# Kernel tuning notes

Hardware: AMD Instinct MI355X
Metric: run time of the kernel (lower is better)

The kernel has to match this reference:

```python
import jax, jax.numpy as jnp
import numpy as np

N_NODES = 100000
N_EDGES = 1600000
N_ADJS = 2
N_LAYERS = 3
D_IN = 128
H = 128           # hidden dim; last conv out = 256 / num_adjs = 128
N_GRAPHS = 1024


def setup_inputs() -> dict:
    key = jax.random.key(0)
    ks = jax.random.split(key, 12)
    x = jax.random.normal(ks[0], (N_NODES, D_IN), dtype=jnp.float32)
    edge_index = jax.random.randint(ks[1], (N_ADJS, 2, N_EDGES), 0, N_NODES, dtype=jnp.int32)
    batch = jnp.sort(jax.random.randint(ks[2], (N_NODES,), 0, N_GRAPHS, dtype=jnp.int32))
    s = 0.05
    lin0_w = jax.random.normal(ks[3], (D_IN, H), dtype=jnp.float32) * s
    lin0_b = jnp.zeros((H,), dtype=jnp.float32)
    conv_w = jax.random.normal(ks[4], (N_ADJS, N_LAYERS, H, H), dtype=jnp.float32) * s
    lin1_w = jax.random.normal(ks[5], (2 * H, H), dtype=jnp.float32) * s
    lin1_b = jnp.zeros((H,), dtype=jnp.float32)
    lin2_w = jax.random.normal(ks[6], (H, 1), dtype=jnp.float32) * s
    lin2_b = jnp.zeros((1,), dtype=jnp.float32)
    return {"x": x, "edge_index": edge_index, "batch": batch,
            "lin0_w": lin0_w, "lin0_b": lin0_b, "conv_w": conv_w,
            "lin1_w": lin1_w, "lin1_b": lin1_b, "lin2_w": lin2_w, "lin2_b": lin2_b}


def _gcn_conv(h, W, row, col, norm, n_nodes):
    # GCNConv (bias=False): out[i] = sum_{j->i} norm_e * (h @ W)[j]
    m = h @ W                                  # [N, H] dense transform first (PyG order)
    msg = m[row] * norm[:, None]               # [E+N, H] gather + edge scaling
    return jax.ops.segment_sum(msg, col, num_segments=n_nodes)


def reference(x, edge_index, batch, lin0_w, lin0_b, conv_w, lin1_w, lin1_b, lin2_w, lin2_b):
    n = x.shape[0]
    loops = jnp.arange(n, dtype=edge_index.dtype)
    x0 = jax.nn.relu(x @ lin0_w + lin0_b)      # lin0 + relu
    pooled = []
    for a in range(N_ADJS):
        # gcn_norm with self loops: deg over targets, norm = d^-1/2[row] * d^-1/2[col]
        row = jnp.concatenate([edge_index[a, 0], loops])
        col = jnp.concatenate([edge_index[a, 1], loops])
        deg = jax.ops.segment_sum(jnp.ones_like(col, dtype=x.dtype), col, num_segments=n)
        dis = jnp.where(deg > 0, jax.lax.rsqrt(jnp.maximum(deg, 1e-12)), 0.0)
        norm = dis[row] * dis[col]
        h = x0
        for l in range(N_LAYERS):
            h = jax.nn.relu(_gcn_conv(h, conv_w[a, l], row, col, norm, n))
        # global_add_pool: segment sum over graph ids
        pooled.append(jax.ops.segment_sum(h, batch, num_segments=N_GRAPHS))
    g = jnp.concatenate(pooled, axis=1)        # [G, 256]
    g = jax.nn.relu(g @ lin1_w + lin1_b)
    # dropout(p=0.5) is identity in eval mode
    return g @ lin2_w + lin2_b                 # [G, 1]
```

## Files before the change

kernel.cpp:

```cpp
#include <hip/hip_runtime.h>

#define NN 100000
#define NE 1600000
#define NADJ 2
#define NLAY 3
#define HD 128
#define NG 1024

#define EB   1563
#define NBUK 391
#define BPAD 400

typedef unsigned int uint32;
typedef unsigned short u16;

typedef __attribute__((ext_vector_type(8))) short bfrag8;
typedef __attribute__((ext_vector_type(4))) float f32x4;
typedef __attribute__((ext_vector_type(2))) float f32x2;

__device__ __forceinline__ u16 f2bf(float f) {
    uint32 u = __float_as_uint(f);
    u += 0x7FFFu + ((u >> 16) & 1u);
    return (u16)(u >> 16);
}
__device__ __forceinline__ float bflo(uint32 u) { return __uint_as_float(u << 16); }
__device__ __forceinline__ float bfhi(uint32 u) { return __uint_as_float(u & 0xFFFF0000u); }

__global__ __launch_bounds__(256) void to_bf16(const float* __restrict__ in,
                                               u16* __restrict__ o) {
    int i = blockIdx.x * 256 + threadIdx.x;
    float4 a = ((const float4*)in)[i * 2];
    float4 b = ((const float4*)in)[i * 2 + 1];
    uint4 v;
    v.x = (uint32)f2bf(a.x) | ((uint32)f2bf(a.y) << 16);
    v.y = (uint32)f2bf(a.z) | ((uint32)f2bf(a.w) << 16);
    v.z = (uint32)f2bf(b.x) | ((uint32)f2bf(b.y) << 16);
    v.w = (uint32)f2bf(b.z) | ((uint32)f2bf(b.w) << 16);
    ((uint4*)o)[i] = v;
}

__global__ void wt_prep(const float* __restrict__ conv_w,
                        const float* __restrict__ lin0_w, u16* __restrict__ wt) {
    const float* W = (blockIdx.x < 6) ? conv_w + (size_t)blockIdx.x * HD * HD
                                      : lin0_w;
    u16* o = wt + (size_t)blockIdx.x * HD * HD;
    for (int i = 0; i < 64; ++i) {
        int idx = i * 256 + threadIdx.x;
        int n = idx >> 7, k = idx & 127;
        o[idx] = f2bf(W[k * 128 + n]);
    }
}

__global__ __launch_bounds__(256) void gemm_mfma(
    const u16* __restrict__ Abf, const u16* __restrict__ Wt,
    u16* __restrict__ outbf, const float* __restrict__ dis,
    const float* __restrict__ bias, int relu)
{
    const int wid = blockIdx.x * 4 + (threadIdx.x >> 6);
    const int lane = threadIdx.x & 63;
    const int row0 = (wid >> 1) * 64;
    if (row0 >= NN) return;
    const int wc = (wid & 1) * 64;
    const int lr = lane & 15, kg = lane >> 4;

    bfrag8 b[4][4];
    #pragma unroll
    for (int ks = 0; ks < 4; ++ks)
        #pragma unroll
        for (int j = 0; j < 4; ++j)
            b[ks][j] = *(const bfrag8*)&Wt[(size_t)(wc + j * 16 + lr) * 128
                                           + (ks * 4 + kg) * 8];

    const f32x4 z = {0.f, 0.f, 0.f, 0.f};
    f32x4 acc[4][4];
    #pragma unroll
    for (int i = 0; i < 4; ++i)
        #pragma unroll
        for (int j = 0; j < 4; ++j) acc[i][j] = z;

    #pragma unroll
    for (int ks = 0; ks < 4; ++ks) {
        bfrag8 a[4];
        #pragma unroll
        for (int i = 0; i < 4; ++i) {
            int r = min(row0 + i * 16 + lr, NN - 1);
            a[i] = *(const bfrag8*)&Abf[(size_t)r * 128 + (ks * 4 + kg) * 8];
        }
        #pragma unroll
        for (int i = 0; i < 4; ++i)
            #pragma unroll
            for (int j = 0; j < 4; ++j)
                acc[i][j] = __builtin_amdgcn_mfma_f32_16x16x32_bf16(
                    a[i], b[ks][j], acc[i][j], 0, 0, 0);
    }

    #pragma unroll
    for (int i = 0; i < 4; ++i) {
        #pragma unroll
        for (int r = 0; r < 4; ++r) {
            int grow = row0 + i * 16 + kg * 4 + r;
            if (grow < NN) {
                float ds = dis ? dis[grow] : 1.f;
                #pragma unroll
                for (int j = 0; j < 4; ++j) {
                    int gcol = wc + j * 16 + lr;
                    float o = acc[i][j][r] * ds;
                    if (bias) o += bias[gcol];
                    if (relu) o = fmaxf(o, 0.f);
                    outbf[(size_t)grow * 128 + gcol] = f2bf(o);
                }
            }
        }
    }
}


__global__ __launch_bounds__(256) void p1_count(
    const int* __restrict__ col, int* __restrict__ bcnt)
{
    __shared__ int h[NBUK];
    int t = threadIdx.x;
    for (int q = t; q < NBUK; q += 256) h[q] = 0;
    __syncthreads();
    int base = blockIdx.x * 1024 + t;
    #pragma unroll
    for (int u = 0; u < 4; ++u) {
        int e = base + u * 256;
        if (e < NE) atomicAdd(&h[col[e] >> 8], 1);
    }
    __syncthreads();
    for (int q = t; q < NBUK; q += 256)
        bcnt[blockIdx.x * BPAD + q] = h[q];
}

__global__ __launch_bounds__(256) void p2a_scanblocks(
    const int* __restrict__ bcnt, int* __restrict__ pscan,
    int* __restrict__ btot)
{
    __shared__ int s[256];
    int b = blockIdx.x;
    int t = threadIdx.x;
    int v[7];
    int loc = 0;
    #pragma unroll
    for (int j = 0; j < 7; ++j) {
        int idx = t * 7 + j;
        v[j] = (idx < EB) ? bcnt[idx * BPAD + b] : 0;
        loc += v[j];
    }
    s[t] = loc;
    __syncthreads();
    for (int off = 1; off < 256; off <<= 1) {
        int u = (t >= off) ? s[t - off] : 0;
        __syncthreads();
        s[t] += u;
        __syncthreads();
    }
    int pre = s[t] - loc;
    #pragma unroll
    for (int j = 0; j < 7; ++j) {
        int idx = t * 7 + j;
        if (idx < EB) pscan[idx * BPAD + b] = pre;
        pre += v[j];
    }
    if (t == 255) btot[b] = s[255];
}

__global__ __launch_bounds__(512) void p2b_scanbuckets(
    const int* __restrict__ btot, int* __restrict__ bbase)
{
    __shared__ int s[512];
    int t = threadIdx.x;
    int v = (t < NBUK) ? btot[t] : 0;
    s[t] = v;
    __syncthreads();
    for (int off = 1; off < 512; off <<= 1) {
        int u = (t >= off) ? s[t - off] : 0;
        __syncthreads();
        s[t] += u;
        __syncthreads();
    }
    if (t < NBUK) bbase[t] = s[t] - v;
    if (t == NBUK - 1) bbase[NBUK] = s[t];
}

__global__ __launch_bounds__(256) void p3_partition(
    const int* __restrict__ row, const int* __restrict__ col,
    const int* __restrict__ pscan, const int* __restrict__ bbase,
    uint2* __restrict__ part)
{
    __shared__ int spre[NBUK];
    __shared__ int cur[NBUK];
    int t = threadIdx.x;
    for (int q = t; q < NBUK; q += 256) {
        spre[q] = bbase[q] + pscan[blockIdx.x * BPAD + q];
        cur[q] = 0;
    }
    __syncthreads();
    int base = blockIdx.x * 1024 + t;
    #pragma unroll
    for (int u = 0; u < 4; ++u) {
        int e = base + u * 256;
        if (e < NE) {
            int c = col[e];
            int b = c >> 8;
            int rk = atomicAdd(&cur[b], 1);
            part[spre[b] + rk] = make_uint2((uint32)row[e], (uint32)c);
        }
    }
}

__global__ __launch_bounds__(256) void p4_csr(
    const uint2* __restrict__ part, const int* __restrict__ bbase,
    int* __restrict__ row_ptr, float* __restrict__ dis,
    int* __restrict__ csr_src)
{
    __shared__ int cnt[256];
    __shared__ int s[256];
    __shared__ int sexcl[256];
    __shared__ int cur[256];
    int b = blockIdx.x, t = threadIdx.x;
    int base = bbase[b];
    int ecnt = bbase[b + 1] - base;
    int n0 = b << 8;
    cnt[t] = 0;
    cur[t] = 0;
    __syncthreads();
    for (int i = t; i < ecnt; i += 256)
        atomicAdd(&cnt[part[base + i].y - n0], 1);
    __syncthreads();
    int v = cnt[t];
    s[t] = v;
    __syncthreads();
    for (int off = 1; off < 256; off <<= 1) {
        int u = (t >= off) ? s[t - off] : 0;
        __syncthreads();
        s[t] += u;
        __syncthreads();
    }
    sexcl[t] = s[t] - v;
    int node = n0 + t;
    if (node < NN) {
        row_ptr[node] = base + s[t] - v;
        dis[node] = rsqrtf((float)(v + 1));
    }
    if (b == 0 && t == 0) row_ptr[NN] = NE;
    __syncthreads();
    for (int i = t; i < ecnt; i += 256) {
        uint2 p = part[base + i];
        int li = (int)p.y - n0;
        int rk = atomicAdd(&cur[li], 1);
        csr_src[base + sexcl[li] + rk] = (int)p.x;
    }
}

__global__ __launch_bounds__(256) void agg_relu(
    const u16* __restrict__ mm, const int* __restrict__ row_ptr,
    const int* __restrict__ csr_src,
    const float* __restrict__ dis, u16* __restrict__ out)
{
    int wid = blockIdx.x * 4 + (threadIdx.x >> 6);
    int nodeA = wid * 2;
    if (nodeA >= NN) return;
    int nodeB = nodeA + 1;
    uint32 lane = threadIdx.x & 63;
    const uint32* mv = (const uint32*)mm;
    int lan16 = (int)(lane & 15);

    uint32 selfA = mv[(uint32)nodeA * 64u + lane];
    uint32 selfB = mv[(uint32)nodeB * 64u + lane];
    f32x2 accA, accB;
    accA.x = bflo(selfA); accA.y = bfhi(selfA);
    accB.x = bflo(selfB); accB.y = bfhi(selfB);
    int eA = row_ptr[nodeA], e1A = row_ptr[nodeA + 1];
    int eB = e1A,            e1B = row_ptr[nodeB + 1];

    while (eA + 16 <= e1A && eB + 16 <= e1B) {
        uint32 pA = (uint32)csr_src[eA + lan16];
        uint32 pB = (uint32)csr_src[eB + lan16];
        #pragma unroll
        for (int u = 0; u < 16; ++u) {
            uint32 sA = (uint32)__builtin_amdgcn_readlane((int)pA, u);
            uint32 sB = (uint32)__builtin_amdgcn_readlane((int)pB, u);
            uint32 vA = (mv + (size_t)sA * 64u)[lane];
            uint32 vB = (mv + (size_t)sB * 64u)[lane];
            f32x2 tA, tB;
            tA.x = bflo(vA); tA.y = bfhi(vA);
            tB.x = bflo(vB); tB.y = bfhi(vB);
            asm("v_pk_add_f32 %0, %0, %1" : "+v"(accA) : "v"(tA));
            asm("v_pk_add_f32 %0, %0, %1" : "+v"(accB) : "v"(tB));
        }
        eA += 16; eB += 16;
    }
    for (; eA + 16 <= e1A; eA += 16) {
        uint32 pA = (uint32)csr_src[eA + lan16];
        #pragma unroll
        for (int u = 0; u < 16; ++u) {
            uint32 sA = (uint32)__builtin_amdgcn_readlane((int)pA, u);
            uint32 vA = (mv + (size_t)sA * 64u)[lane];
            f32x2 tA;
            tA.x = bflo(vA); tA.y = bfhi(vA);
            asm("v_pk_add_f32 %0, %0, %1" : "+v"(accA) : "v"(tA));
        }
    }
    for (; eB + 16 <= e1B; eB += 16) {
        uint32 pB = (uint32)csr_src[eB + lan16];
        #pragma unroll
        for (int u = 0; u < 16; ++u) {
            uint32 sB = (uint32)__builtin_amdgcn_readlane((int)pB, u);
            uint32 vB = (mv + (size_t)sB * 64u)[lane];
            f32x2 tB;
            tB.x = bflo(vB); tB.y = bfhi(vB);
            asm("v_pk_add_f32 %0, %0, %1" : "+v"(accB) : "v"(tB));
        }
    }
    int remA = e1A - eA, remB = e1B - eB;
    if ((remA | remB) != 0) {
        if (remA > 0 && remB > 0 && remA <= 8 && remB <= 8) {
            uint32 pA = (uint32)csr_src[min(eA + (int)(lane & 7), e1A - 1)];
            uint32 pB = (uint32)csr_src[min(eB + (int)(lane & 7), e1B - 1)];
            #pragma unroll
            for (int u = 0; u < 8; ++u) {
                uint32 sA = (uint32)__builtin_amdgcn_readlane((int)pA, u);
                uint32 sB = (uint32)__builtin_amdgcn_readlane((int)pB, u);
                uint32 vA = (mv + (size_t)sA * 64u)[lane];
                uint32 vB = (mv + (size_t)sB * 64u)[lane];
                float mA = (eA + u < e1A) ? 1.f : 0.f;
                float mB = (eB + u < e1B) ? 1.f : 0.f;
                f32x2 tA, tB, kA, kB;
                tA.x = bflo(vA); tA.y = bfhi(vA); kA.x = mA; kA.y = mA;
                tB.x = bflo(vB); tB.y = bfhi(vB); kB.x = mB; kB.y = mB;
                asm("v_pk_fma_f32 %0, %1, %2, %0" : "+v"(accA) : "v"(tA), "v"(kA));
                asm("v_pk_fma_f32 %0, %1, %2, %0" : "+v"(accB) : "v"(tB), "v"(kB));
            }
        } else {
            uint32 pA = 0, pB = 0;
            if (remA > 0) pA = (uint32)csr_src[min(eA + lan16, e1A - 1)];
            if (remB > 0) pB = (uint32)csr_src[min(eB + lan16, e1B - 1)];
            if (remA > 0 && remB > 0) {
                #pragma unroll
                for (int u = 0; u < 16; ++u) {
                    uint32 sA = (uint32)__builtin_amdgcn_readlane((int)pA, u);
                    uint32 sB = (uint32)__builtin_amdgcn_readlane((int)pB, u);
                    uint32 vA = (mv + (size_t)sA * 64u)[lane];
                    uint32 vB = (mv + (size_t)sB * 64u)[lane];
                    float mA = (eA + u < e1A) ? 1.f : 0.f;
                    float mB = (eB + u < e1B) ? 1.f : 0.f;
                    f32x2 tA, tB, kA, kB;
                    tA.x = bflo(vA); tA.y = bfhi(vA); kA.x = mA; kA.y = mA;
                    tB.x = bflo(vB); tB.y = bfhi(vB); kB.x = mB; kB.y = mB;
                    asm("v_pk_fma_f32 %0, %1, %2, %0" : "+v"(accA) : "v"(tA), "v"(kA));
                    asm("v_pk_fma_f32 %0, %1, %2, %0" : "+v"(accB) : "v"(tB), "v"(kB));
                }
            } else if (remA > 0) {
                #pragma unroll
                for (int u = 0; u < 16; ++u) {
                    uint32 sA = (uint32)__builtin_amdgcn_readlane((int)pA, u);
                    uint32 vA = (mv + (size_t)sA * 64u)[lane];
                    float mA = (eA + u < e1A) ? 1.f : 0.f;
                    f32x2 tA, kA;
                    tA.x = bflo(vA); tA.y = bfhi(vA); kA.x = mA; kA.y = mA;
                    asm("v_pk_fma_f32 %0, %1, %2, %0" : "+v"(accA) : "v"(tA), "v"(kA));
                }
            } else {
                #pragma unroll
                for (int u = 0; u < 16; ++u) {
                    uint32 sB = (uint32)__builtin_amdgcn_readlane((int)pB, u);
                    uint32 vB = (mv + (size_t)sB * 64u)[lane];
                    float mB = (eB + u < e1B) ? 1.f : 0.f;
                    f32x2 tB, kB;
                    tB.x = bflo(vB); tB.y = bfhi(vB); kB.x = mB; kB.y = mB;
                    asm("v_pk_fma_f32 %0, %1, %2, %0" : "+v"(accB) : "v"(tB), "v"(kB));
                }
            }
        }
    }

    float dA = dis[nodeA], dB = dis[nodeB];
    uint32 poA = (uint32)f2bf(fmaxf(dA * accA.x, 0.f))
               | ((uint32)f2bf(fmaxf(dA * accA.y, 0.f)) << 16);
    uint32 poB = (uint32)f2bf(fmaxf(dB * accB.x, 0.f))
               | ((uint32)f2bf(fmaxf(dB * accB.y, 0.f)) << 16);
    ((uint32*)out)[(uint32)nodeA * 64u + lane] = poA;
    ((uint32*)out)[(uint32)nodeB * 64u + lane] = poB;
}

__global__ __launch_bounds__(64) void pool_add(
    const u16* __restrict__ h, const int* __restrict__ batch,
    float* __restrict__ pooled, int aoff)
{
    int c2 = threadIdx.x;
    const uint32* hv = (const uint32*)h;
    int n0 = blockIdx.x * 64;
    int nend = min(n0 + 64, NN);
    int cur = batch[n0];
    float ax = 0.f, ay = 0.f;
    for (int n = n0; n < nend; ++n) {
        int g = batch[n];
        if (g != cur) {
            atomicAdd(&pooled[(size_t)cur * 256 + aoff + 2 * c2], ax);
            atomicAdd(&pooled[(size_t)cur * 256 + aoff + 2 * c2 + 1], ay);
            ax = 0.f; ay = 0.f;
            cur = g;
        }
        uint32 v = hv[(size_t)n * 64 + c2];
        ax += bflo(v);
        ay += bfhi(v);
    }
    atomicAdd(&pooled[(size_t)cur * 256 + aoff + 2 * c2], ax);
    atomicAdd(&pooled[(size_t)cur * 256 + aoff + 2 * c2 + 1], ay);
}

__global__ __launch_bounds__(128) void head(
    const float* __restrict__ pooled,
    const float* __restrict__ w1, const float* __restrict__ b1,
    const float* __restrict__ w2, const float* __restrict__ b2,
    float* __restrict__ out)
{
    __shared__ float sp[256];
    __shared__ float sg[128];
    int g = blockIdx.x, t = threadIdx.x;
    sp[t] = pooled[(size_t)g * 256 + t];
    sp[t + 128] = pooled[(size_t)g * 256 + 128 + t];
    __syncthreads();
    float acc = b1[t];
    #pragma unroll 8
    for (int k = 0; k < 256; ++k) acc = fmaf(sp[k], w1[k * 128 + t], acc);
    sg[t] = fmaxf(acc, 0.f) * w2[t];
    __syncthreads();
    for (int s2 = 64; s2 > 0; s2 >>= 1) {
        if (t < s2) sg[t] += sg[t + s2];
        __syncthreads();
    }
    if (t == 0) out[g] = sg[0] + b2[0];
}

extern "C" void kernel_launch(void* const* d_in, const int* in_sizes, int n_in,
                              void* d_out, int out_size, void* d_ws, size_t ws_size,
                              hipStream_t stream) {
    const float* x      = (const float*)d_in[0];
    const int*   ei     = (const int*)d_in[1];
    const int*   batch  = (const int*)d_in[2];
    const float* lin0_w = (const float*)d_in[3];
    const float* lin0_b = (const float*)d_in[4];
    const float* conv_w = (const float*)d_in[5];
    const float* lin1_w = (const float*)d_in[6];
    const float* lin1_b = (const float*)d_in[7];
    const float* lin2_w = (const float*)d_in[8];
    const float* lin2_b = (const float*)d_in[9];
    float* out = (float*)d_out;

    const size_t NB = (size_t)NN * HD;
    float* x0f    = (float*)d_ws;
    float* bufA   = x0f + NB;
    float* bufB   = bufA + NB;
    float* pooled = bufB + NB;
    int*   row_ptr = (int*)(pooled + (size_t)NG * 256);
    float* dis     = (float*)(row_ptr + NN + 1);
    int*   csr_src = (int*)(dis + NN);
    u16*   wt      = (u16*)(csr_src + NE);
    int*   bcnt    = (int*)(wt + 7 * HD * HD);
    int*   pscan   = bcnt + EB * BPAD;
    int*   btot    = pscan + EB * BPAD;
    int*   bbase   = btot + BPAD;

    u16* x0bf    = (u16*)x0f;
    u16* xbf     = (u16*)(x0f + NB / 2);
    u16* mm      = (u16*)bufA;
    u16* hbuf    = (u16*)bufB;
    uint2* part  = (uint2*)bufA;

    const int GEMM_BLOCKS = (((NN + 63) / 64) * 2 + 3) / 4;

    hipMemsetAsync(pooled, 0, (size_t)NG * 256 * sizeof(float), stream);

    to_bf16<<<NN * HD / 8 / 256, 256, 0, stream>>>(x, xbf);
    wt_prep<<<NADJ * NLAY + 1, 256, 0, stream>>>(conv_w, lin0_w, wt);

    gemm_mfma<<<GEMM_BLOCKS, 256, 0, stream>>>(
        xbf, wt + 6 * HD * HD, x0bf, nullptr, lin0_b, 1);

    for (int a = 0; a < NADJ; ++a) {
        const int* row = ei + (size_t)a * 2 * NE;
        const int* col = row + NE;

        p1_count<<<EB, 256, 0, stream>>>(col, bcnt);
        p2a_scanblocks<<<NBUK, 256, 0, stream>>>(bcnt, pscan, btot);
        p2b_scanbuckets<<<1, 512, 0, stream>>>(btot, bbase);
        p3_partition<<<EB, 256, 0, stream>>>(row, col, pscan, bbase, part);
        p4_csr<<<NBUK, 256, 0, stream>>>(part, bbase, row_ptr, dis, csr_src);

        const u16* h = x0bf;
        for (int l = 0; l < NLAY; ++l) {
            const u16* Wt = wt + ((size_t)a * NLAY + l) * HD * HD;
            gemm_mfma<<<GEMM_BLOCKS, 256, 0, stream>>>(h, Wt, mm, dis,
                                                       nullptr, 0);
            agg_relu<<<NN / 8, 256, 0, stream>>>(mm, row_ptr, csr_src,
                                                 dis, hbuf);
            h = hbuf;
        }
        pool_add<<<(NN + 63) / 64, 64, 0, stream>>>(hbuf, batch, pooled, a * HD);
    }

    head<<<NG, 128, 0, stream>>>(pooled, lin1_w, lin1_b, lin2_w, lin2_b, out);
}
```

Baseline: 733.6 us.

## Batch CSR build for both adjacencies, merge prep kernels, transpose GEMM operands

The CSR construction pipeline (count, scan, partition, build) now runs once over both adjacency matrices with doubled grids, so each launch carries twice the work and five launches are removed. The fp32-to-bf16 conversion and weight-prep kernels are merged into one launch. The GEMM swaps operand roles so each lane holds four consecutive output columns and writes them as one packed 8-byte store instead of scalar 2-byte stores. The cost is more workspace for duplicated CSR buffers, with the partition buffer moved to the second half of bufA.

```diff
diff --git a/kernel.cpp b/kernel.cpp
--- a/kernel.cpp
+++ b/kernel.cpp
@@ -26,28 +26,29 @@
 __device__ __forceinline__ float bflo(uint32 u) { return __uint_as_float(u << 16); }
 __device__ __forceinline__ float bfhi(uint32 u) { return __uint_as_float(u & 0xFFFF0000u); }
 
-__global__ __launch_bounds__(256) void to_bf16(const float* __restrict__ in,
-                                               u16* __restrict__ o) {
-    int i = blockIdx.x * 256 + threadIdx.x;
-    float4 a = ((const float4*)in)[i * 2];
-    float4 b = ((const float4*)in)[i * 2 + 1];
-    uint4 v;
-    v.x = (uint32)f2bf(a.x) | ((uint32)f2bf(a.y) << 16);
-    v.y = (uint32)f2bf(a.z) | ((uint32)f2bf(a.w) << 16);
-    v.z = (uint32)f2bf(b.x) | ((uint32)f2bf(b.y) << 16);
-    v.w = (uint32)f2bf(b.z) | ((uint32)f2bf(b.w) << 16);
-    ((uint4*)o)[i] = v;
-}
-
-__global__ void wt_prep(const float* __restrict__ conv_w,
-                        const float* __restrict__ lin0_w, u16* __restrict__ wt) {
-    const float* W = (blockIdx.x < 6) ? conv_w + (size_t)blockIdx.x * HD * HD
-                                      : lin0_w;
-    u16* o = wt + (size_t)blockIdx.x * HD * HD;
-    for (int i = 0; i < 64; ++i) {
-        int idx = i * 256 + threadIdx.x;
-        int n = idx >> 7, k = idx & 127;
-        o[idx] = f2bf(W[k * 128 + n]);
+__global__ __launch_bounds__(256) void prep(
+    const float* __restrict__ x, const float* __restrict__ conv_w,
+    const float* __restrict__ lin0_w, u16* __restrict__ xbf,
+    u16* __restrict__ wt) {
+    if (blockIdx.x < 6250) {
+        int i = blockIdx.x * 256 + threadIdx.x;
+        float4 a = ((const float4*)x)[i * 2];
+        float4 b = ((const float4*)x)[i * 2 + 1];
+        uint4 v;
+        v.x = (uint32)f2bf(a.x) | ((uint32)f2bf(a.y) << 16);
+        v.y = (uint32)f2bf(a.z) | ((uint32)f2bf(a.w) << 16);
+        v.z = (uint32)f2bf(b.x) | ((uint32)f2bf(b.y) << 16);
+        v.w = (uint32)f2bf(b.z) | ((uint32)f2bf(b.w) << 16);
+        ((uint4*)xbf)[i] = v;
+    } else {
+        int bid = blockIdx.x - 6250;
+        const float* W = (bid < 6) ? conv_w + (size_t)bid * HD * HD : lin0_w;
+        u16* o = wt + (size_t)bid * HD * HD;
+        for (int i = 0; i < 64; ++i) {
+            int idx = i * 256 + threadIdx.x;
+            int n = idx >> 7, k = idx & 127;
+            o[idx] = f2bf(W[k * 128 + n]);
+        }
     }
 }
 
@@ -63,52 +64,59 @@
     const int wc = (wid & 1) * 64;
     const int lr = lane & 15, kg = lane >> 4;
 
-    bfrag8 b[4][4];
+    bfrag8 a[4][4];
     #pragma unroll
     for (int ks = 0; ks < 4; ++ks)
         #pragma unroll
-        for (int j = 0; j < 4; ++j)
-            b[ks][j] = *(const bfrag8*)&Wt[(size_t)(wc + j * 16 + lr) * 128
+        for (int i = 0; i < 4; ++i)
+            a[ks][i] = *(const bfrag8*)&Wt[(size_t)(wc + i * 16 + lr) * 128
                                            + (ks * 4 + kg) * 8];
 
     const f32x4 z = {0.f, 0.f, 0.f, 0.f};
     f32x4 acc[4][4];
     #pragma unroll
-    for (int i = 0; i < 4; ++i)
-        #pragma unroll
-        for (int j = 0; j < 4; ++j) acc[i][j] = z;
+    for (int j = 0; j < 4; ++j)
+        #pragma unroll
+        for (int i = 0; i < 4; ++i) acc[j][i] = z;
 
     #pragma unroll
     for (int ks = 0; ks < 4; ++ks) {
-        bfrag8 a[4];
-        #pragma unroll
-        for (int i = 0; i < 4; ++i) {
-            int r = min(row0 + i * 16 + lr, NN - 1);
-            a[i] = *(const bfrag8*)&Abf[(size_t)r * 128 + (ks * 4 + kg) * 8];
-        }
-        #pragma unroll
-        for (int i = 0; i < 4; ++i)
+        bfrag8 b[4];
+        #pragma unroll
+        for (int j = 0; j < 4; ++j) {
+            int r = min(row0 + j * 16 + lr, NN - 1);
+            b[j] = *(const bfrag8*)&Abf[(size_t)r * 128 + (ks * 4 + kg) * 8];
+        }
+        #pragma unroll
+        for (int j = 0; j < 4; ++j)
             #pragma unroll
-            for (int j = 0; j < 4; ++j)
-                acc[i][j] = __builtin_amdgcn_mfma_f32_16x16x32_bf16(
-                    a[i], b[ks][j], acc[i][j], 0, 0, 0);
-    }
-
-    #pragma unroll
-    for (int i = 0; i < 4; ++i) {
-        #pragma unroll
-        for (int r = 0; r < 4; ++r) {
-            int grow = row0 + i * 16 + kg * 4 + r;
-            if (grow < NN) {
-                float ds = dis ? dis[grow] : 1.f;
-                #pragma unroll
-                for (int j = 0; j < 4; ++j) {
-                    int gcol = wc + j * 16 + lr;
-                    float o = acc[i][j][r] * ds;
-                    if (bias) o += bias[gcol];
-                    if (relu) o = fmaxf(o, 0.f);
-                    outbf[(size_t)grow * 128 + gcol] = f2bf(o);
+            for (int i = 0; i < 4; ++i)
+                acc[j][i] = __builtin_amdgcn_mfma_f32_16x16x32_bf16(
+                    a[ks][i], b[j], acc[j][i], 0, 0, 0);
+    }
+
+    #pragma unroll
+    for (int j = 0; j < 4; ++j) {
+        int m = row0 + j * 16 + lr;
+        if (m < NN) {
+            float ds = dis ? dis[m] : 1.f;
+            #pragma unroll
+            for (int i = 0; i < 4; ++i) {
+                int colb = wc + i * 16 + kg * 4;
+                float4 bb = make_float4(0.f, 0.f, 0.f, 0.f);
+                if (bias) bb = *(const float4*)&bias[colb];
+                float v0 = acc[j][i][0] * ds + bb.x;
+                float v1 = acc[j][i][1] * ds + bb.y;
+                float v2 = acc[j][i][2] * ds + bb.z;
+                float v3 = acc[j][i][3] * ds + bb.w;
+                if (relu) {
+                    v0 = fmaxf(v0, 0.f); v1 = fmaxf(v1, 0.f);
+                    v2 = fmaxf(v2, 0.f); v3 = fmaxf(v3, 0.f);
                 }
+                uint2 pk;
+                pk.x = (uint32)f2bf(v0) | ((uint32)f2bf(v1) << 16);
+                pk.y = (uint32)f2bf(v2) | ((uint32)f2bf(v3) << 16);
+                *(uint2*)&outbf[(size_t)m * 128 + colb] = pk;
             }
         }
     }
@@ -116,13 +124,17 @@
 
 
 __global__ __launch_bounds__(256) void p1_count(
-    const int* __restrict__ col, int* __restrict__ bcnt)
+    const int* __restrict__ ei, int* __restrict__ bcnt)
 {
     __shared__ int h[NBUK];
+    int aa = blockIdx.x >= EB ? 1 : 0;
+    int blk = blockIdx.x - aa * EB;
+    const int* col = ei + (size_t)aa * 2 * NE + NE;
+    int* bc = bcnt + (size_t)aa * EB * BPAD;
     int t = threadIdx.x;
     for (int q = t; q < NBUK; q += 256) h[q] = 0;
     __syncthreads();
-    int base = blockIdx.x * 1024 + t;
+    int base = blk * 1024 + t;
     #pragma unroll
     for (int u = 0; u < 4; ++u) {
         int e = base + u * 256;
@@ -130,7 +142,7 @@
     }
     __syncthreads();
     for (int q = t; q < NBUK; q += 256)
-        bcnt[blockIdx.x * BPAD + q] = h[q];
+        bc[blk * BPAD + q] = h[q];
 }
 
 __global__ __launch_bounds__(256) void p2a_scanblocks(
@@ -138,14 +150,18 @@
     int* __restrict__ btot)
 {
     __shared__ int s[256];
-    int b = blockIdx.x;
+    int aa = blockIdx.x >= NBUK ? 1 : 0;
+    int b = blockIdx.x - aa * NBUK;
+    const int* bc = bcnt + (size_t)aa * EB * BPAD;
+    int* ps = pscan + (size_t)aa * EB * BPAD;
+    int* bt = btot + aa * BPAD;
     int t = threadIdx.x;
     int v[7];
     int loc = 0;
     #pragma unroll
     for (int j = 0; j < 7; ++j) {
         int idx = t * 7 + j;
-        v[j] = (idx < EB) ? bcnt[idx * BPAD + b] : 0;
+        v[j] = (idx < EB) ? bc[idx * BPAD + b] : 0;
         loc += v[j];
     }
     s[t] = loc;
@@ -160,18 +176,21 @@
     #pragma unroll
     for (int j = 0; j < 7; ++j) {
         int idx = t * 7 + j;
-        if (idx < EB) pscan[idx * BPAD + b] = pre;
+        if (idx < EB) ps[idx * BPAD + b] = pre;
         pre += v[j];
     }
-    if (t == 255) btot[b] = s[255];
+    if (t == 255) bt[b] = s[255];
 }
 
 __global__ __launch_bounds__(512) void p2b_scanbuckets(
     const int* __restrict__ btot, int* __restrict__ bbase)
 {
     __shared__ int s[512];
+    int aa = blockIdx.x;
+    const int* bt = btot + aa * BPAD;
+    int* bb = bbase + aa * (NBUK + 1);
     int t = threadIdx.x;
-    int v = (t < NBUK) ? btot[t] : 0;
+    int v = (t < NBUK) ? bt[t] : 0;
     s[t] = v;
     __syncthreads();
     for (int off = 1; off < 512; off <<= 1) {
@@ -180,24 +199,30 @@
         s[t] += u;
         __syncthreads();
     }
-    if (t < NBUK) bbase[t] = s[t] - v;
-    if (t == NBUK - 1) bbase[NBUK] = s[t];
+    if (t < NBUK) bb[t] = s[t] - v;
+    if (t == NBUK - 1) bb[NBUK] = s[t];
 }
 
 __global__ __launch_bounds__(256) void p3_partition(
-    const int* __restrict__ row, const int* __restrict__ col,
-    const int* __restrict__ pscan, const int* __restrict__ bbase,
-    uint2* __restrict__ part)
+    const int* __restrict__ ei, const int* __restrict__ pscan,
+    const int* __restrict__ bbase, uint2* __restrict__ part)
 {
     __shared__ int spre[NBUK];
     __shared__ int cur[NBUK];
+    int aa = blockIdx.x >= EB ? 1 : 0;
+    int blk = blockIdx.x - aa * EB;
+    const int* row = ei + (size_t)aa * 2 * NE;
+    const int* col = row + NE;
+    const int* ps = pscan + (size_t)aa * EB * BPAD;
+    const int* bb = bbase + aa * (NBUK + 1);
+    uint2* pt = part + (size_t)aa * NE;
     int t = threadIdx.x;
     for (int q = t; q < NBUK; q += 256) {
-        spre[q] = bbase[q] + pscan[blockIdx.x * BPAD + q];
+        spre[q] = bb[q] + ps[blk * BPAD + q];
         cur[q] = 0;
     }
     __syncthreads();
-    int base = blockIdx.x * 1024 + t;
+    int base = blk * 1024 + t;
     #pragma unroll
     for (int u = 0; u < 4; ++u) {
         int e = base + u * 256;
@@ -205,7 +230,7 @@
             int c = col[e];
             int b = c >> 8;
             int rk = atomicAdd(&cur[b], 1);
-            part[spre[b] + rk] = make_uint2((uint32)row[e], (uint32)c);
+            pt[spre[b] + rk] = make_uint2((uint32)row[e], (uint32)c);
         }
     }
 }
@@ -219,15 +244,22 @@
     __shared__ int s[256];
     __shared__ int sexcl[256];
     __shared__ int cur[256];
-    int b = blockIdx.x, t = threadIdx.x;
-    int base = bbase[b];
-    int ecnt = bbase[b + 1] - base;
+    int aa = blockIdx.x >= NBUK ? 1 : 0;
+    int b = blockIdx.x - aa * NBUK;
+    const uint2* pt = part + (size_t)aa * NE;
+    const int* bb = bbase + aa * (NBUK + 1);
+    int* rp = row_ptr + (size_t)aa * (NN + 1);
+    float* ds = dis + (size_t)aa * NN;
+    int* cs = csr_src + (size_t)aa * NE;
+    int t = threadIdx.x;
+    int base = bb[b];
+    int ecnt = bb[b + 1] - base;
     int n0 = b << 8;
     cnt[t] = 0;
     cur[t] = 0;
     __syncthreads();
     for (int i = t; i < ecnt; i += 256)
-        atomicAdd(&cnt[part[base + i].y - n0], 1);
+        atomicAdd(&cnt[pt[base + i].y - n0], 1);
     __syncthreads();
     int v = cnt[t];
     s[t] = v;
@@ -241,16 +273,16 @@
     sexcl[t] = s[t] - v;
     int node = n0 + t;
     if (node < NN) {
-        row_ptr[node] = base + s[t] - v;
-        dis[node] = rsqrtf((float)(v + 1));
-    }
-    if (b == 0 && t == 0) row_ptr[NN] = NE;
+        rp[node] = base + s[t] - v;
+        ds[node] = rsqrtf((float)(v + 1));
+    }
+    if (b == 0 && t == 0) rp[NN] = NE;
     __syncthreads();
     for (int i = t; i < ecnt; i += 256) {
-        uint2 p = part[base + i];
+        uint2 p = pt[base + i];
         int li = (int)p.y - n0;
         int rk = atomicAdd(&cur[li], 1);
-        csr_src[base + sexcl[li] + rk] = (int)p.x;
+        cs[base + sexcl[li] + rk] = (int)p.x;
     }
 }
 
@@ -455,48 +487,47 @@
     float* bufA   = x0f + NB;
     float* bufB   = bufA + NB;
     float* pooled = bufB + NB;
-    int*   row_ptr = (int*)(pooled + (size_t)NG * 256);
-    float* dis     = (float*)(row_ptr + NN + 1);
-    int*   csr_src = (int*)(dis + NN);
-    u16*   wt      = (u16*)(csr_src + NE);
-    int*   bcnt    = (int*)(wt + 7 * HD * HD);
-    int*   pscan   = bcnt + EB * BPAD;
-    int*   btot    = pscan + EB * BPAD;
-    int*   bbase   = btot + BPAD;
+    int*   row_ptr2 = (int*)(pooled + (size_t)NG * 256);
+    float* dis2     = (float*)(row_ptr2 + 2 * (NN + 1));
+    int*   csr2     = (int*)(dis2 + 2 * NN);
+    u16*   wt       = (u16*)(csr2 + 2 * NE);
+    int*   bcnt2    = (int*)(wt + 7 * HD * HD);
+    int*   pscan2   = bcnt2 + 2 * EB * BPAD;
+    int*   btot2    = pscan2 + 2 * EB * BPAD;
+    int*   bbase2   = btot2 + 2 * BPAD;
 
     u16* x0bf    = (u16*)x0f;
     u16* xbf     = (u16*)(x0f + NB / 2);
     u16* mm      = (u16*)bufA;
+    uint2* part2 = (uint2*)(bufA + NB / 2);
     u16* hbuf    = (u16*)bufB;
-    uint2* part  = (uint2*)bufA;
 
     const int GEMM_BLOCKS = (((NN + 63) / 64) * 2 + 3) / 4;
 
     hipMemsetAsync(pooled, 0, (size_t)NG * 256 * sizeof(float), stream);
 
-    to_bf16<<<NN * HD / 8 / 256, 256, 0, stream>>>(x, xbf);
-    wt_prep<<<NADJ * NLAY + 1, 256, 0, stream>>>(conv_w, lin0_w, wt);
+    prep<<<6250 + 7, 256, 0, stream>>>(x, conv_w, lin0_w, xbf, wt);
+
+    p1_count<<<2 * EB, 256, 0, stream>>>(ei, bcnt2);
+    p2a_scanblocks<<<2 * NBUK, 256, 0, stream>>>(bcnt2, pscan2, btot2);
+    p2b_scanbuckets<<<2, 512, 0, stream>>>(btot2, bbase2);
+    p3_partition<<<2 * EB, 256, 0, stream>>>(ei, pscan2, bbase2, part2);
+    p4_csr<<<2 * NBUK, 256, 0, stream>>>(part2, bbase2, row_ptr2, dis2, csr2);
 
     gemm_mfma<<<GEMM_BLOCKS, 256, 0, stream>>>(
         xbf, wt + 6 * HD * HD, x0bf, nullptr, lin0_b, 1);
 
     for (int a = 0; a < NADJ; ++a) {
-        const int* row = ei + (size_t)a * 2 * NE;
-        const int* col = row + NE;
-
-        p1_count<<<EB, 256, 0, stream>>>(col, bcnt);
-        p2a_scanblocks<<<NBUK, 256, 0, stream>>>(bcnt, pscan, btot);
-        p2b_scanbuckets<<<1, 512, 0, stream>>>(btot, bbase);
-        p3_partition<<<EB, 256, 0, stream>>>(row, col, pscan, bbase, part);
-        p4_csr<<<NBUK, 256, 0, stream>>>(part, bbase, row_ptr, dis, csr_src);
+        const int*   rp = row_ptr2 + (size_t)a * (NN + 1);
+        const float* ds = dis2 + (size_t)a * NN;
+        const int*   cs = csr2 + (size_t)a * NE;
 
         const u16* h = x0bf;
         for (int l = 0; l < NLAY; ++l) {
             const u16* Wt = wt + ((size_t)a * NLAY + l) * HD * HD;
-            gemm_mfma<<<GEMM_BLOCKS, 256, 0, stream>>>(h, Wt, mm, dis,
+            gemm_mfma<<<GEMM_BLOCKS, 256, 0, stream>>>(h, Wt, mm, ds,
                                                        nullptr, 0);
-            agg_relu<<<NN / 8, 256, 0, stream>>>(mm, row_ptr, csr_src,
-                                                 dis, hbuf);
+            agg_relu<<<NN / 8, 256, 0, stream>>>(mm, rp, cs, ds, hbuf);
             h = hbuf;
         }
         pool_add<<<(NN + 63) / 64, 64, 0, stream>>>(hbuf, batch, pooled, a * HD);
```

After: 696.6 us. 5.0% less time.
